# Optimization experiments

Hardware: AMD Instinct MI355X
Metric: run time of the kernel (lower is better)

Reference implementation:

```python
import jax, jax.numpy as jnp
import numpy as np

B, N, D, H = 8, 1024, 512, 512  # batch, nodes/graph, input dim, hidden/output dim
NEG_SLOPE = 0.2


def _gatv2_layer(x, src, dst, Wl, bl, Wr, br, a, bias, nseg):
    """PyG GATv2Conv (heads=1, add_self_loops=False, eval mode -> no dropout).
    message j->i: alpha_ij = softmax_i( a . leaky_relu(xl[j] + xr[i]) ); out[i] = sum_j alpha_ij * xl[j] + bias
    """
    xl = x @ Wl + bl              # [nseg, H] source transform
    xr = x @ Wr + br              # [nseg, H] target transform
    e = jax.nn.leaky_relu(xl[src] + xr[dst], NEG_SLOPE) @ a  # [E] raw scores
    m = jax.lax.stop_gradient(jax.ops.segment_max(e, dst, num_segments=nseg))
    ex = jnp.exp(e - m[dst])
    s = jax.ops.segment_sum(ex, dst, num_segments=nseg)
    alpha = ex / s[dst]                                       # segment softmax over incoming edges
    out = jax.ops.segment_sum(alpha[:, None] * xl[src], dst, num_segments=nseg)
    return out + bias


def setup_inputs() -> dict:
    key = jax.random.key(0)
    rng = np.random.RandomState(0)
    # random per-graph adjacency, avg degree ~16; block-diagonal edge extraction
    adj_np = (rng.rand(B, N, N) < (16.0 / N))
    srcs, dsts = [], []
    for b in range(B):  # matches torch.nonzero(big_adj).t(): row=src, col=dst
        r, c = np.nonzero(adj_np[b])
        srcs.append(r + b * N)
        dsts.append(c + b * N)
    edge_index = jnp.asarray(np.stack([np.concatenate(srcs), np.concatenate(dsts)]).astype(np.int32))

    ks = jax.random.split(key, 32)
    def lin(k, fi, fo):
        return (jax.random.normal(k, (fi, fo), jnp.float32) / np.sqrt(fi)).astype(jnp.float32)
    inp = {
        "batch_graph": jax.random.normal(ks[0], (B, N, D), jnp.float32),
        "adj": jnp.asarray(adj_np.astype(np.float32)),
        "edge_index": edge_index,
    }
    dims = [(D, H), (H, H), (H, H)]
    for i, (fi, fo) in enumerate(dims, start=1):
        k = jax.random.split(ks[i], 6)
        inp[f"Wl{i}"] = lin(k[0], fi, fo)
        inp[f"bl{i}"] = jnp.zeros((fo,), jnp.float32)
        inp[f"Wr{i}"] = lin(k[1], fi, fo)
        inp[f"br{i}"] = jnp.zeros((fo,), jnp.float32)
        inp[f"a{i}"] = (jax.random.normal(k[2], (fo,), jnp.float32) / np.sqrt(fo)).astype(jnp.float32)
        inp[f"bias{i}"] = jnp.zeros((fo,), jnp.float32)
    return inp


def reference(batch_graph, adj, edge_index,
              Wl1, bl1, Wr1, br1, a1, bias1,
              Wl2, bl2, Wr2, br2, a2, bias2,
              Wl3, bl3, Wr3, br3, a3, bias3):
    b, n, d = batch_graph.shape
    nseg = b * n
    x = batch_graph.reshape(nseg, d)
    src, dst = edge_index[0], edge_index[1]
    x = _gatv2_layer(x, src, dst, Wl1, bl1, Wr1, br1, a1, bias1, nseg)  # graph_norm = Identity
    x = _gatv2_layer(x, src, dst, Wl2, bl2, Wr2, br2, a2, bias2, nseg)
    x = _gatv2_layer(x, src, dst, Wl3, bl3, Wr3, br3, a3, bias3, nseg)
    return x.reshape(b, n, -1)
```

## Files before the change

### kernel.cpp

```cpp
#include <hip/hip_runtime.h>
#include <math.h>

#define MTOT 8192
#define HD   512
#define NEG  0.2f

typedef __attribute__((ext_vector_type(8))) short bf16x8;
typedef __attribute__((ext_vector_type(4))) float floatx4;

__device__ inline unsigned short f2bf(float f) {
    unsigned int u = __float_as_uint(f);
    unsigned int r = (u + 0x7FFFu + ((u >> 16) & 1u)) >> 16;
    return (unsigned short)r;
}
__device__ inline float bf2f(unsigned short h) {
    return __uint_as_float(((unsigned int)h) << 16);
}


__global__ void zero_ints(int* p, int n) {
    int i = blockIdx.x * 256 + threadIdx.x;
    if (i < n) p[i] = 0;
}

__global__ void count_deg(const int* __restrict__ dst, int* __restrict__ deg, int E) {
    int i = blockIdx.x * 256 + threadIdx.x;
    if (i < E) atomicAdd(&deg[dst[i]], 1);
}

__global__ __launch_bounds__(1024) void scan_offsets(const int* __restrict__ deg,
                                                     int* __restrict__ offs,
                                                     int* __restrict__ cursor) {
    __shared__ int part[1024];
    int tid = threadIdx.x;
    int base = tid * 8;
    int v[8]; int s = 0;
    #pragma unroll
    for (int i = 0; i < 8; ++i) { v[i] = deg[base + i]; s += v[i]; }
    part[tid] = s;
    __syncthreads();
    for (int off = 1; off < 1024; off <<= 1) {
        int t = (tid >= off) ? part[tid - off] : 0;
        __syncthreads();
        part[tid] += t;
        __syncthreads();
    }
    int run = (tid == 0) ? 0 : part[tid - 1];
    #pragma unroll
    for (int i = 0; i < 8; ++i) {
        offs[base + i] = run;
        cursor[base + i] = run;
        run += v[i];
    }
    if (tid == 1023) offs[MTOT] = run;
}

__global__ void scatter_edges(const int* __restrict__ src, const int* __restrict__ dst,
                              int* __restrict__ cursor, int* __restrict__ csr_src, int E) {
    int i = blockIdx.x * 256 + threadIdx.x;
    if (i < E) {
        int p = atomicAdd(&cursor[dst[i]], 1);
        csr_src[p] = src[i];
    }
}


__global__ __launch_bounds__(256) void act_convert(const float* __restrict__ X,
                                                   unsigned short* __restrict__ Ahi,
                                                   unsigned short* __restrict__ Alo) {
    int i = (blockIdx.x * 256 + threadIdx.x) * 4;
    float4 v = *(const float4*)(X + i);
    ushort4 h, l;
    h.x = f2bf(v.x); l.x = f2bf(v.x - bf2f(h.x));
    h.y = f2bf(v.y); l.y = f2bf(v.y - bf2f(h.y));
    h.z = f2bf(v.z); l.z = f2bf(v.z - bf2f(h.z));
    h.w = f2bf(v.w); l.w = f2bf(v.w - bf2f(h.w));
    *(ushort4*)(Ahi + i) = h;
    *(ushort4*)(Alo + i) = l;
}

__global__ __launch_bounds__(256) void wt_convert(const float* __restrict__ W,
                                                  unsigned short* __restrict__ Whi,
                                                  unsigned short* __restrict__ Wlo) {
    __shared__ float t[32][33];
    int bx = blockIdx.x * 32;
    int by = blockIdx.y * 32;
    int tx = threadIdx.x, ty = threadIdx.y;
    for (int i = ty; i < 32; i += 8)
        t[i][tx] = W[(size_t)(by + i) * 512 + bx + tx];
    __syncthreads();
    for (int i = ty; i < 32; i += 8) {
        float v = t[tx][i];
        unsigned short h = f2bf(v);
        unsigned short l = f2bf(v - bf2f(h));
        Whi[(size_t)(bx + i) * 512 + by + tx] = h;
        Wlo[(size_t)(bx + i) * 512 + by + tx] = l;
    }
}


__global__ __launch_bounds__(256) void gemm_mfma_dual(
    const unsigned short* __restrict__ Ahi, const unsigned short* __restrict__ Alo,
    const unsigned short* __restrict__ Bhi_l, const unsigned short* __restrict__ Blo_l,
    const unsigned short* __restrict__ Bhi_r, const unsigned short* __restrict__ Blo_r,
    const float* __restrict__ bias_l, const float* __restrict__ bias_r,
    float* __restrict__ Cl, float* __restrict__ Cr)
{
    const unsigned short* Bhi = blockIdx.z ? Bhi_r : Bhi_l;
    const unsigned short* Blo = blockIdx.z ? Blo_r : Blo_l;
    const float* bias         = blockIdx.z ? bias_r : bias_l;
    float* C                  = blockIdx.z ? Cr : Cl;

    __shared__ __align__(16) unsigned short lds[4 * 128 * 32];

    int tid = threadIdx.x;
    int wave = tid >> 6, lane = tid & 63;
    int bm = blockIdx.y * 128, bn = blockIdx.x * 128;

    const unsigned short* gsrc[4] = {Ahi, Alo, Bhi, Blo};
    int rowbase[4] = {bm, bm, bn, bn};

    const unsigned short* gbase =
        gsrc[wave] + (size_t)(rowbase[wave] + (lane >> 2)) * 512 + (lane & 3) * 8;

    floatx4 acc[4][4] = {};

    int wm = wave & 1, wn = wave >> 1;
    int lr = lane & 15, lq = lane >> 4;

    for (int k0 = 0; k0 < 512; k0 += 32) {
        const unsigned short* g = gbase + k0;
        #pragma unroll
        for (int rg = 0; rg < 8; ++rg) {
            __builtin_amdgcn_global_load_lds(
                (const __attribute__((address_space(1))) unsigned int*)(g + (size_t)rg * 16 * 512),
                (__attribute__((address_space(3))) unsigned int*)(&lds[wave * 4096 + rg * 512]),
                16, 0, 0);
        }
        __syncthreads();

        bf16x8 ah[4], al[4], bh[4], bl_[4];
        #pragma unroll
        for (int i = 0; i < 4; ++i) {
            int mrow = wm * 64 + i * 16 + lr;
            ah[i]  = *(const bf16x8*)&lds[0 * 4096 + mrow * 32 + lq * 8];
            al[i]  = *(const bf16x8*)&lds[1 * 4096 + mrow * 32 + lq * 8];
            int nrow = wn * 64 + i * 16 + lr;
            bh[i]  = *(const bf16x8*)&lds[2 * 4096 + nrow * 32 + lq * 8];
            bl_[i] = *(const bf16x8*)&lds[3 * 4096 + nrow * 32 + lq * 8];
        }
        #pragma unroll
        for (int i = 0; i < 4; ++i)
            #pragma unroll
            for (int j = 0; j < 4; ++j) {
                acc[i][j] = __builtin_amdgcn_mfma_f32_16x16x32_bf16(ah[i], bh[j],  acc[i][j], 0, 0, 0);
                acc[i][j] = __builtin_amdgcn_mfma_f32_16x16x32_bf16(ah[i], bl_[j], acc[i][j], 0, 0, 0);
                acc[i][j] = __builtin_amdgcn_mfma_f32_16x16x32_bf16(al[i], bh[j],  acc[i][j], 0, 0, 0);
            }
        __syncthreads();
    }

    #pragma unroll
    for (int j = 0; j < 4; ++j) {
        int n = bn + wn * 64 + j * 16 + lr;
        float bv = bias[n];
        #pragma unroll
        for (int i = 0; i < 4; ++i) {
            int mbase = bm + wm * 64 + i * 16 + lq * 4;
            #pragma unroll
            for (int r = 0; r < 4; ++r)
                C[(size_t)(mbase + r) * 512 + n] = acc[i][j][r] + bv;
        }
    }
}


#define DOT8(pe, x0, x1)                                        \
    { float t;                                                  \
      t = x0.x + r0.x; pe  = a0.x * (t > 0.f ? t : NEG * t);    \
      t = x0.y + r0.y; pe += a0.y * (t > 0.f ? t : NEG * t);    \
      t = x0.z + r0.z; pe += a0.z * (t > 0.f ? t : NEG * t);    \
      t = x0.w + r0.w; pe += a0.w * (t > 0.f ? t : NEG * t);    \
      t = x1.x + r1.x; pe += a1.x * (t > 0.f ? t : NEG * t);    \
      t = x1.y + r1.y; pe += a1.y * (t > 0.f ? t : NEG * t);    \
      t = x1.z + r1.z; pe += a1.z * (t > 0.f ? t : NEG * t);    \
      t = x1.w + r1.w; pe += a1.w * (t > 0.f ? t : NEG * t); }

#define UPDATE(m, l, A0, A1, pe, x0, x1)                        \
    { float nm = fmaxf(m, pe);                                  \
      float sc = __expf(m - nm);                                \
      float w  = __expf(pe - nm);                               \
      l = l * sc + w;                                           \
      A0.x = A0.x * sc + w * x0.x; A0.y = A0.y * sc + w * x0.y; \
      A0.z = A0.z * sc + w * x0.z; A0.w = A0.w * sc + w * x0.w; \
      A1.x = A1.x * sc + w * x1.x; A1.y = A1.y * sc + w * x1.y; \
      A1.z = A1.z * sc + w * x1.z; A1.w = A1.w * sc + w * x1.w; \
      m = nm; }

__global__ __launch_bounds__(256) void gat_aggregate(
    const float* __restrict__ xl, const float* __restrict__ xr,
    const float* __restrict__ avec, const float* __restrict__ bias,
    const int* __restrict__ offs, const int* __restrict__ csr_src,
    float* __restrict__ out,
    unsigned short* __restrict__ Ohi,
    unsigned short* __restrict__ Olo,
    int write_fp32) {
    int gid = blockIdx.x;
    int node = ((gid & 7) << 10) + ((gid >> 3) << 2) + (threadIdx.x >> 6);
    int lane = threadIdx.x & 63;
    int h0 = lane << 2;

    float4 a0 = *(const float4*)(avec + h0);
    float4 a1 = *(const float4*)(avec + 256 + h0);
    const float* xrrow = xr + (size_t)node * HD;
    float4 r0 = *(const float4*)(xrrow + h0);
    float4 r1 = *(const float4*)(xrrow + 256 + h0);

    const float NEGM = -1e30f;
    float m0 = NEGM, m1 = NEGM, m2 = NEGM, m3 = NEGM;
    float l0 = 0.f, l1 = 0.f, l2 = 0.f, l3 = 0.f;
    float4 z = {0.f, 0.f, 0.f, 0.f};
    float4 A00 = z, A01 = z, A10 = z, A11 = z, A20 = z, A21 = z, A30 = z, A31 = z;

    int beg = offs[node], end = offs[node + 1];
    int p = beg;
    for (; p + 4 <= end; p += 4) {
        int j0 = csr_src[p + 0], j1 = csr_src[p + 1];
        int j2 = csr_src[p + 2], j3 = csr_src[p + 3];
        const float* q0 = xl + (size_t)j0 * HD;
        const float* q1 = xl + (size_t)j1 * HD;
        const float* q2 = xl + (size_t)j2 * HD;
        const float* q3 = xl + (size_t)j3 * HD;
        float4 x00 = *(const float4*)(q0 + h0), x01 = *(const float4*)(q0 + 256 + h0);
        float4 x10 = *(const float4*)(q1 + h0), x11 = *(const float4*)(q1 + 256 + h0);
        float4 x20 = *(const float4*)(q2 + h0), x21 = *(const float4*)(q2 + 256 + h0);
        float4 x30 = *(const float4*)(q3 + h0), x31 = *(const float4*)(q3 + 256 + h0);

        float pe0, pe1, pe2, pe3;
        DOT8(pe0, x00, x01);
        DOT8(pe1, x10, x11);
        DOT8(pe2, x20, x21);
        DOT8(pe3, x30, x31);
        #pragma unroll
        for (int off = 32; off; off >>= 1) {
            pe0 += __shfl_xor(pe0, off, 64);
            pe1 += __shfl_xor(pe1, off, 64);
            pe2 += __shfl_xor(pe2, off, 64);
            pe3 += __shfl_xor(pe3, off, 64);
        }
        UPDATE(m0, l0, A00, A01, pe0, x00, x01);
        UPDATE(m1, l1, A10, A11, pe1, x10, x11);
        UPDATE(m2, l2, A20, A21, pe2, x20, x21);
        UPDATE(m3, l3, A30, A31, pe3, x30, x31);
    }
    for (; p < end; ++p) {
        int j = csr_src[p];
        const float* q = xl + (size_t)j * HD;
        float4 x0 = *(const float4*)(q + h0), x1 = *(const float4*)(q + 256 + h0);
        float pe;
        DOT8(pe, x0, x1);
        #pragma unroll
        for (int off = 32; off; off >>= 1) pe += __shfl_xor(pe, off, 64);
        UPDATE(m0, l0, A00, A01, pe, x0, x1);
    }

    float M = fmaxf(fmaxf(m0, m1), fmaxf(m2, m3));
    float s0 = __expf(m0 - M), s1 = __expf(m1 - M);
    float s2 = __expf(m2 - M), s3 = __expf(m3 - M);
    float l = l0 * s0 + l1 * s1 + l2 * s2 + l3 * s3;
    float4 acc0, acc1;
    acc0.x = A00.x * s0 + A10.x * s1 + A20.x * s2 + A30.x * s3;
    acc0.y = A00.y * s0 + A10.y * s1 + A20.y * s2 + A30.y * s3;
    acc0.z = A00.z * s0 + A10.z * s1 + A20.z * s2 + A30.z * s3;
    acc0.w = A00.w * s0 + A10.w * s1 + A20.w * s2 + A30.w * s3;
    acc1.x = A01.x * s0 + A11.x * s1 + A21.x * s2 + A31.x * s3;
    acc1.y = A01.y * s0 + A11.y * s1 + A21.y * s2 + A31.y * s3;
    acc1.z = A01.z * s0 + A11.z * s1 + A21.z * s2 + A31.z * s3;
    acc1.w = A01.w * s0 + A11.w * s1 + A21.w * s2 + A31.w * s3;

    float inv = (l > 0.f) ? 1.f / l : 0.f;
    float4 b0 = *(const float4*)(bias + h0);
    float4 b1 = *(const float4*)(bias + 256 + h0);
    float4 o0 = {acc0.x * inv + b0.x, acc0.y * inv + b0.y,
                 acc0.z * inv + b0.z, acc0.w * inv + b0.w};
    float4 o1 = {acc1.x * inv + b1.x, acc1.y * inv + b1.y,
                 acc1.z * inv + b1.z, acc1.w * inv + b1.w};

    if (write_fp32) {
        float* orow = out + (size_t)node * HD;
        *(float4*)(orow + h0) = o0;
        *(float4*)(orow + 256 + h0) = o1;
    } else {
        size_t rb = (size_t)node * HD;
        ushort4 h, lo;
        h.x = f2bf(o0.x); lo.x = f2bf(o0.x - bf2f(h.x));
        h.y = f2bf(o0.y); lo.y = f2bf(o0.y - bf2f(h.y));
        h.z = f2bf(o0.z); lo.z = f2bf(o0.z - bf2f(h.z));
        h.w = f2bf(o0.w); lo.w = f2bf(o0.w - bf2f(h.w));
        *(ushort4*)(Ohi + rb + h0) = h;
        *(ushort4*)(Olo + rb + h0) = lo;
        h.x = f2bf(o1.x); lo.x = f2bf(o1.x - bf2f(h.x));
        h.y = f2bf(o1.y); lo.y = f2bf(o1.y - bf2f(h.y));
        h.z = f2bf(o1.z); lo.z = f2bf(o1.z - bf2f(h.z));
        h.w = f2bf(o1.w); lo.w = f2bf(o1.w - bf2f(h.w));
        *(ushort4*)(Ohi + rb + 256 + h0) = h;
        *(ushort4*)(Olo + rb + 256 + h0) = lo;
    }
}


extern "C" void kernel_launch(void* const* d_in, const int* in_sizes, int n_in,
                              void* d_out, int out_size, void* d_ws, size_t ws_size,
                              hipStream_t stream) {
    const float* x0 = (const float*)d_in[0];
    const int* eidx = (const int*)d_in[2];
    int E = in_sizes[2] / 2;
    const int* esrc = eidx;
    const int* edst = eidx + E;

    const float* Wl[3] = {(const float*)d_in[3],  (const float*)d_in[9],  (const float*)d_in[15]};
    const float* bl[3] = {(const float*)d_in[4],  (const float*)d_in[10], (const float*)d_in[16]};
    const float* Wr[3] = {(const float*)d_in[5],  (const float*)d_in[11], (const float*)d_in[17]};
    const float* br[3] = {(const float*)d_in[6],  (const float*)d_in[12], (const float*)d_in[18]};
    const float* av[3] = {(const float*)d_in[7],  (const float*)d_in[13], (const float*)d_in[19]};
    const float* bs[3] = {(const float*)d_in[8],  (const float*)d_in[14], (const float*)d_in[20]};

    char* w = (char*)d_ws;
    unsigned short* Ahi = (unsigned short*)w; w += (size_t)MTOT * HD * 2;
    unsigned short* Alo = (unsigned short*)w; w += (size_t)MTOT * HD * 2;
    unsigned short* Wt[12];
    for (int i = 0; i < 12; ++i) { Wt[i] = (unsigned short*)w; w += (size_t)HD * HD * 2; }
    float* xl = (float*)w; w += (size_t)MTOT * HD * 4;
    float* xr = (float*)w; w += (size_t)MTOT * HD * 4;
    int* deg    = (int*)w;
    int* offs   = deg + MTOT;
    int* cursor = offs + MTOT + 8;
    int* csr    = cursor + MTOT;

    dim3 wtg(16, 16), wtb(32, 8);
    for (int L = 0; L < 3; ++L) {
        wt_convert<<<wtg, wtb, 0, stream>>>(Wl[L], Wt[L * 4 + 0], Wt[L * 4 + 1]);
        wt_convert<<<wtg, wtb, 0, stream>>>(Wr[L], Wt[L * 4 + 2], Wt[L * 4 + 3]);
    }

    zero_ints<<<(MTOT + 255) / 256, 256, 0, stream>>>(deg, MTOT);
    count_deg<<<(E + 255) / 256, 256, 0, stream>>>(edst, deg, E);
    scan_offsets<<<1, 1024, 0, stream>>>(deg, offs, cursor);
    scatter_edges<<<(E + 255) / 256, 256, 0, stream>>>(esrc, edst, cursor, csr, E);

    act_convert<<<(MTOT * HD / 4 + 255) / 256, 256, 0, stream>>>(x0, Ahi, Alo);

    dim3 ggrid(HD / 128, MTOT / 128, 2);
    for (int L = 0; L < 3; ++L) {
        gemm_mfma_dual<<<ggrid, 256, 0, stream>>>(Ahi, Alo,
                                                  Wt[L * 4 + 0], Wt[L * 4 + 1],
                                                  Wt[L * 4 + 2], Wt[L * 4 + 3],
                                                  bl[L], br[L], xl, xr);
        int last = (L == 2);
        gat_aggregate<<<MTOT / 4, 256, 0, stream>>>(xl, xr, av[L], bs[L], offs, csr,
                                                    last ? (float*)d_out : nullptr,
                                                    last ? nullptr : Ahi,
                                                    last ? nullptr : Alo,
                                                    last);
    }
}
```

Before: 371.7 us.

## Split GAT aggregation into edge-parallel score kernel and softmax-apply kernel

Result: no change. 368.9 us (-0.8%).

```diff
diff --git a/kernel.cpp b/kernel.cpp
--- a/kernel.cpp
+++ b/kernel.cpp
@@ -4,6 +4,7 @@
 #define MTOT 8192
 #define HD   512
 #define NEG  0.2f
+#define BPG  512
 
 typedef __attribute__((ext_vector_type(8))) short bf16x8;
 typedef __attribute__((ext_vector_type(4))) float floatx4;
@@ -56,11 +57,14 @@
 }
 
 __global__ void scatter_edges(const int* __restrict__ src, const int* __restrict__ dst,
-                              int* __restrict__ cursor, int* __restrict__ csr_src, int E) {
+                              int* __restrict__ cursor, int* __restrict__ csr_src,
+                              int* __restrict__ csr_dst, int E) {
     int i = blockIdx.x * 256 + threadIdx.x;
     if (i < E) {
-        int p = atomicAdd(&cursor[dst[i]], 1);
+        int d = dst[i];
+        int p = atomicAdd(&cursor[d], 1);
         csr_src[p] = src[i];
+        csr_dst[p] = d;
     }
 }
 
@@ -79,22 +83,32 @@
     *(ushort4*)(Alo + i) = l;
 }
 
-__global__ __launch_bounds__(256) void wt_convert(const float* __restrict__ W,
-                                                  unsigned short* __restrict__ Whi,
-                                                  unsigned short* __restrict__ Wlo) {
+__global__ __launch_bounds__(256) void wt_convert_all(
+    const float* __restrict__ W0, const float* __restrict__ W1,
+    const float* __restrict__ W2, const float* __restrict__ W3,
+    const float* __restrict__ W4, const float* __restrict__ W5,
+    unsigned short* __restrict__ wtbase) {
+    int z = blockIdx.z;
+    const float* W = (z == 0) ? W0 : (z == 1) ? W1 : (z == 2) ? W2
+                   : (z == 3) ? W3 : (z == 4) ? W4 : W5;
+    int L = z >> 1, lr = z & 1;
+    const size_t SZ = (size_t)HD * HD;
+    unsigned short* Whi = wtbase + (L * 4 + lr * 2) * SZ;
+    unsigned short* Wlo = Whi + SZ;
+
     __shared__ float t[32][33];
     int bx = blockIdx.x * 32;
     int by = blockIdx.y * 32;
-    int tx = threadIdx.x, ty = threadIdx.y;
+    int tx = threadIdx.x & 31, ty = threadIdx.x >> 5;
     for (int i = ty; i < 32; i += 8)
-        t[i][tx] = W[(size_t)(by + i) * 512 + bx + tx];
+        t[i][tx] = W[(size_t)(by + i) * HD + bx + tx];
     __syncthreads();
     for (int i = ty; i < 32; i += 8) {
         float v = t[tx][i];
         unsigned short h = f2bf(v);
         unsigned short l = f2bf(v - bf2f(h));
-        Whi[(size_t)(bx + i) * 512 + by + tx] = h;
-        Wlo[(size_t)(bx + i) * 512 + by + tx] = l;
+        Whi[(size_t)(bx + i) * HD + by + tx] = h;
+        Wlo[(size_t)(bx + i) * HD + by + tx] = l;
     }
 }
 
@@ -175,58 +189,91 @@
 }
 
 
-#define DOT8(pe, x0, x1)                                        \
-    { float t;                                                  \
-      t = x0.x + r0.x; pe  = a0.x * (t > 0.f ? t : NEG * t);    \
-      t = x0.y + r0.y; pe += a0.y * (t > 0.f ? t : NEG * t);    \
-      t = x0.z + r0.z; pe += a0.z * (t > 0.f ? t : NEG * t);    \
-      t = x0.w + r0.w; pe += a0.w * (t > 0.f ? t : NEG * t);    \
-      t = x1.x + r1.x; pe += a1.x * (t > 0.f ? t : NEG * t);    \
-      t = x1.y + r1.y; pe += a1.y * (t > 0.f ? t : NEG * t);    \
-      t = x1.z + r1.z; pe += a1.z * (t > 0.f ? t : NEG * t);    \
-      t = x1.w + r1.w; pe += a1.w * (t > 0.f ? t : NEG * t); }
-
-#define UPDATE(m, l, A0, A1, pe, x0, x1)                        \
-    { float nm = fmaxf(m, pe);                                  \
-      float sc = __expf(m - nm);                                \
-      float w  = __expf(pe - nm);                               \
-      l = l * sc + w;                                           \
-      A0.x = A0.x * sc + w * x0.x; A0.y = A0.y * sc + w * x0.y; \
-      A0.z = A0.z * sc + w * x0.z; A0.w = A0.w * sc + w * x0.w; \
-      A1.x = A1.x * sc + w * x1.x; A1.y = A1.y * sc + w * x1.y; \
-      A1.z = A1.z * sc + w * x1.z; A1.w = A1.w * sc + w * x1.w; \
-      m = nm; }
-
-__global__ __launch_bounds__(256) void gat_aggregate(
+__global__ __launch_bounds__(256) void edge_scores(
     const float* __restrict__ xl, const float* __restrict__ xr,
-    const float* __restrict__ avec, const float* __restrict__ bias,
+    const float* __restrict__ avec,
     const int* __restrict__ offs, const int* __restrict__ csr_src,
-    float* __restrict__ out,
-    unsigned short* __restrict__ Ohi,
-    unsigned short* __restrict__ Olo,
-    int write_fp32) {
+    const int* __restrict__ csr_dst, float* __restrict__ escore)
+{
+    int g = blockIdx.x & 7;
+    int chunk = blockIdx.x >> 3;
+    int gb = offs[g << 10], ge = offs[(g + 1) << 10];
+    int wave = threadIdx.x >> 6, lane = threadIdx.x & 63;
+    int sub = lane >> 4, flane = lane & 15;
+
+    float4 av[8];
+    #pragma unroll
+    for (int i = 0; i < 8; ++i)
+        av[i] = *(const float4*)(avec + i * 64 + flane * 4);
+
+    for (int base = gb + ((chunk << 2) + wave) * 4; base < ge; base += BPG * 16) {
+        int p = base + sub;
+        bool valid = p < ge;
+        int srcn = valid ? csr_src[p] : 0;
+        int dstn = valid ? csr_dst[p] : 0;
+        const float* xls = xl + (size_t)srcn * HD;
+        const float* xrs = xr + (size_t)dstn * HD;
+
+        float pe = 0.f;
+        #pragma unroll
+        for (int i = 0; i < 8; ++i) {
+            float4 xv = *(const float4*)(xls + i * 64 + flane * 4);
+            float4 rv = *(const float4*)(xrs + i * 64 + flane * 4);
+            float t;
+            t = xv.x + rv.x; pe += av[i].x * (t > 0.f ? t : NEG * t);
+            t = xv.y + rv.y; pe += av[i].y * (t > 0.f ? t : NEG * t);
+            t = xv.z + rv.z; pe += av[i].z * (t > 0.f ? t : NEG * t);
+            t = xv.w + rv.w; pe += av[i].w * (t > 0.f ? t : NEG * t);
+        }
+        pe += __shfl_xor(pe, 1, 64);
+        pe += __shfl_xor(pe, 2, 64);
+        pe += __shfl_xor(pe, 4, 64);
+        pe += __shfl_xor(pe, 8, 64);
+        if (valid && flane == 0) escore[p] = pe;
+    }
+}
+
+
+__global__ __launch_bounds__(256) void gat_apply(
+    const float* __restrict__ xl, const float* __restrict__ escore,
+    const float* __restrict__ bias,
+    const int* __restrict__ offs, const int* __restrict__ csr_src,
+    float* __restrict__ out, unsigned short* __restrict__ Ohi,
+    unsigned short* __restrict__ Olo, int write_fp32)
+{
+    __shared__ float alpha_sh[4][128];
     int gid = blockIdx.x;
     int node = ((gid & 7) << 10) + ((gid >> 3) << 2) + (threadIdx.x >> 6);
+    int wv = threadIdx.x >> 6;
     int lane = threadIdx.x & 63;
     int h0 = lane << 2;
 
-    float4 a0 = *(const float4*)(avec + h0);
-    float4 a1 = *(const float4*)(avec + 256 + h0);
-    const float* xrrow = xr + (size_t)node * HD;
-    float4 r0 = *(const float4*)(xrrow + h0);
-    float4 r1 = *(const float4*)(xrrow + 256 + h0);
-
-    const float NEGM = -1e30f;
-    float m0 = NEGM, m1 = NEGM, m2 = NEGM, m3 = NEGM;
-    float l0 = 0.f, l1 = 0.f, l2 = 0.f, l3 = 0.f;
-    float4 z = {0.f, 0.f, 0.f, 0.f};
-    float4 A00 = z, A01 = z, A10 = z, A11 = z, A20 = z, A21 = z, A30 = z, A31 = z;
-
     int beg = offs[node], end = offs[node + 1];
-    int p = beg;
-    for (; p + 4 <= end; p += 4) {
-        int j0 = csr_src[p + 0], j1 = csr_src[p + 1];
-        int j2 = csr_src[p + 2], j3 = csr_src[p + 3];
+    int deg = end - beg;
+    if (deg > 128) deg = 128;
+
+    float m = -1e30f;
+    for (int i = lane; i < deg; i += 64) m = fmaxf(m, escore[beg + i]);
+    #pragma unroll
+    for (int off = 32; off; off >>= 1) m = fmaxf(m, __shfl_xor(m, off, 64));
+
+    float s = 0.f;
+    for (int i = lane; i < deg; i += 64) {
+        float w = __expf(escore[beg + i] - m);
+        alpha_sh[wv][i] = w;
+        s += w;
+    }
+    #pragma unroll
+    for (int off = 32; off; off >>= 1) s += __shfl_xor(s, off, 64);
+    float inv = (s > 0.f) ? 1.f / s : 0.f;
+
+    float4 acc0 = {0.f, 0.f, 0.f, 0.f}, acc1 = {0.f, 0.f, 0.f, 0.f};
+    int p = 0;
+    for (; p + 4 <= deg; p += 4) {
+        float w0 = alpha_sh[wv][p + 0], w1 = alpha_sh[wv][p + 1];
+        float w2 = alpha_sh[wv][p + 2], w3 = alpha_sh[wv][p + 3];
+        int j0 = csr_src[beg + p + 0], j1 = csr_src[beg + p + 1];
+        int j2 = csr_src[beg + p + 2], j3 = csr_src[beg + p + 3];
         const float* q0 = xl + (size_t)j0 * HD;
         const float* q1 = xl + (size_t)j1 * HD;
         const float* q2 = xl + (size_t)j2 * HD;
@@ -235,50 +282,24 @@
         float4 x10 = *(const float4*)(q1 + h0), x11 = *(const float4*)(q1 + 256 + h0);
         float4 x20 = *(const float4*)(q2 + h0), x21 = *(const float4*)(q2 + 256 + h0);
         float4 x30 = *(const float4*)(q3 + h0), x31 = *(const float4*)(q3 + 256 + h0);
-
-        float pe0, pe1, pe2, pe3;
-        DOT8(pe0, x00, x01);
-        DOT8(pe1, x10, x11);
-        DOT8(pe2, x20, x21);
-        DOT8(pe3, x30, x31);
-        #pragma unroll
-        for (int off = 32; off; off >>= 1) {
-            pe0 += __shfl_xor(pe0, off, 64);
-            pe1 += __shfl_xor(pe1, off, 64);
-            pe2 += __shfl_xor(pe2, off, 64);
-            pe3 += __shfl_xor(pe3, off, 64);
-        }
-        UPDATE(m0, l0, A00, A01, pe0, x00, x01);
-        UPDATE(m1, l1, A10, A11, pe1, x10, x11);
-        UPDATE(m2, l2, A20, A21, pe2, x20, x21);
-        UPDATE(m3, l3, A30, A31, pe3, x30, x31);
-    }
-    for (; p < end; ++p) {
-        int j = csr_src[p];
+        acc0.x += w0 * x00.x + w1 * x10.x + w2 * x20.x + w3 * x30.x;
+        acc0.y += w0 * x00.y + w1 * x10.y + w2 * x20.y + w3 * x30.y;
+        acc0.z += w0 * x00.z + w1 * x10.z + w2 * x20.z + w3 * x30.z;
+        acc0.w += w0 * x00.w + w1 * x10.w + w2 * x20.w + w3 * x30.w;
+        acc1.x += w0 * x01.x + w1 * x11.x + w2 * x21.x + w3 * x31.x;
+        acc1.y += w0 * x01.y + w1 * x11.y + w2 * x21.y + w3 * x31.y;
+        acc1.z += w0 * x01.z + w1 * x11.z + w2 * x21.z + w3 * x31.z;
+        acc1.w += w0 * x01.w + w1 * x11.w + w2 * x21.w + w3 * x31.w;
+    }
+    for (; p < deg; ++p) {
+        float w = alpha_sh[wv][p];
+        int j = csr_src[beg + p];
         const float* q = xl + (size_t)j * HD;
         float4 x0 = *(const float4*)(q + h0), x1 = *(const float4*)(q + 256 + h0);
-        float pe;
-        DOT8(pe, x0, x1);
-        #pragma unroll
-        for (int off = 32; off; off >>= 1) pe += __shfl_xor(pe, off, 64);
-        UPDATE(m0, l0, A00, A01, pe, x0, x1);
-    }
-
-    float M = fmaxf(fmaxf(m0, m1), fmaxf(m2, m3));
-    float s0 = __expf(m0 - M), s1 = __expf(m1 - M);
-    float s2 = __expf(m2 - M), s3 = __expf(m3 - M);
-    float l = l0 * s0 + l1 * s1 + l2 * s2 + l3 * s3;
-    float4 acc0, acc1;
-    acc0.x = A00.x * s0 + A10.x * s1 + A20.x * s2 + A30.x * s3;
-    acc0.y = A00.y * s0 + A10.y * s1 + A20.y * s2 + A30.y * s3;
-    acc0.z = A00.z * s0 + A10.z * s1 + A20.z * s2 + A30.z * s3;
-    acc0.w = A00.w * s0 + A10.w * s1 + A20.w * s2 + A30.w * s3;
-    acc1.x = A01.x * s0 + A11.x * s1 + A21.x * s2 + A31.x * s3;
-    acc1.y = A01.y * s0 + A11.y * s1 + A21.y * s2 + A31.y * s3;
-    acc1.z = A01.z * s0 + A11.z * s1 + A21.z * s2 + A31.z * s3;
-    acc1.w = A01.w * s0 + A11.w * s1 + A21.w * s2 + A31.w * s3;
-
-    float inv = (l > 0.f) ? 1.f / l : 0.f;
+        acc0.x += w * x0.x; acc0.y += w * x0.y; acc0.z += w * x0.z; acc0.w += w * x0.w;
+        acc1.x += w * x1.x; acc1.y += w * x1.y; acc1.z += w * x1.z; acc1.w += w * x1.w;
+    }
+
     float4 b0 = *(const float4*)(bias + h0);
     float4 b1 = *(const float4*)(bias + 256 + h0);
     float4 o0 = {acc0.x * inv + b0.x, acc0.y * inv + b0.y,
@@ -328,39 +349,39 @@
     char* w = (char*)d_ws;
     unsigned short* Ahi = (unsigned short*)w; w += (size_t)MTOT * HD * 2;
     unsigned short* Alo = (unsigned short*)w; w += (size_t)MTOT * HD * 2;
-    unsigned short* Wt[12];
-    for (int i = 0; i < 12; ++i) { Wt[i] = (unsigned short*)w; w += (size_t)HD * HD * 2; }
+    unsigned short* wtbase = (unsigned short*)w; w += 12 * (size_t)HD * HD * 2;
     float* xl = (float*)w; w += (size_t)MTOT * HD * 4;
     float* xr = (float*)w; w += (size_t)MTOT * HD * 4;
+    float* escore = (float*)w; w += (size_t)E * 4;
     int* deg    = (int*)w;
     int* offs   = deg + MTOT;
     int* cursor = offs + MTOT + 8;
     int* csr    = cursor + MTOT;
-
-    dim3 wtg(16, 16), wtb(32, 8);
-    for (int L = 0; L < 3; ++L) {
-        wt_convert<<<wtg, wtb, 0, stream>>>(Wl[L], Wt[L * 4 + 0], Wt[L * 4 + 1]);
-        wt_convert<<<wtg, wtb, 0, stream>>>(Wr[L], Wt[L * 4 + 2], Wt[L * 4 + 3]);
-    }
+    int* csrd   = csr + E;
+    const size_t SZ = (size_t)HD * HD;
+
+    dim3 wtg(16, 16, 6);
+    wt_convert_all<<<wtg, 256, 0, stream>>>(Wl[0], Wr[0], Wl[1], Wr[1], Wl[2], Wr[2], wtbase);
 
     zero_ints<<<(MTOT + 255) / 256, 256, 0, stream>>>(deg, MTOT);
     count_deg<<<(E + 255) / 256, 256, 0, stream>>>(edst, deg, E);
     scan_offsets<<<1, 1024, 0, stream>>>(deg, offs, cursor);
-    scatter_edges<<<(E + 255) / 256, 256, 0, stream>>>(esrc, edst, cursor, csr, E);
+    scatter_edges<<<(E + 255) / 256, 256, 0, stream>>>(esrc, edst, cursor, csr, csrd, E);
 
     act_convert<<<(MTOT * HD / 4 + 255) / 256, 256, 0, stream>>>(x0, Ahi, Alo);
 
     dim3 ggrid(HD / 128, MTOT / 128, 2);
     for (int L = 0; L < 3; ++L) {
         gemm_mfma_dual<<<ggrid, 256, 0, stream>>>(Ahi, Alo,
-                                                  Wt[L * 4 + 0], Wt[L * 4 + 1],
-                                                  Wt[L * 4 + 2], Wt[L * 4 + 3],
-                                                  bl[L], br[L], xl, xr);
+            wtbase + (L * 4 + 0) * SZ, wtbase + (L * 4 + 1) * SZ,
+            wtbase + (L * 4 + 2) * SZ, wtbase + (L * 4 + 3) * SZ,
+            bl[L], br[L], xl, xr);
+        edge_scores<<<8 * BPG, 256, 0, stream>>>(xl, xr, av[L], offs, csr, csrd, escore);
         int last = (L == 2);
-        gat_aggregate<<<MTOT / 4, 256, 0, stream>>>(xl, xr, av[L], bs[L], offs, csr,
-                                                    last ? (float*)d_out : nullptr,
-                                                    last ? nullptr : Ahi,
-                                                    last ? nullptr : Alo,
-                                                    last);
-    }
-}
+        gat_apply<<<MTOT / 4, 256, 0, stream>>>(xl, escore, bs[L], offs, csr,
+                                                last ? (float*)d_out : nullptr,
+                                                last ? nullptr : Ahi,
+                                                last ? nullptr : Alo,
+                                                last);
+    }
+}
```
